# Kernel optimization log

Measured on AMD Instinct MI355X. Metric: run time of the kernel, lower is better.

## Reference

```python
import jax, jax.numpy as jnp
import numpy as np

N = 524288      # total nodes across batched subgraphs
E = 4194304     # total edges (avg degree ~8)
B = 4096        # number of subgraphs (links)
H = 32          # hidden_dim
L = 3           # num_layers
K = 30          # sort-pool k
MAXZ = 1000     # max DRNL label
EPS = 1e-5      # BatchNorm eps


def setup_inputs() -> dict:
    key = jax.random.key(0)
    ks = jax.random.split(key, 12)
    x_z = jax.random.randint(ks[0], (N,), 0, MAXZ + 1, dtype=jnp.int32)
    edge_index = jax.random.randint(ks[1], (2, E), 0, N, dtype=jnp.int32)
    batch = jnp.sort(jax.random.randint(ks[2], (N,), 0, B, dtype=jnp.int32))
    # parameters
    emb = jax.random.normal(ks[3], (MAXZ + 1, H), jnp.float32) * 0.1
    Wc = jax.random.normal(ks[4], (L, H, H), jnp.float32) * (1.0 / np.sqrt(H))
    bc = jnp.zeros((L, H), jnp.float32)
    gamma = jnp.ones((L, H), jnp.float32)
    beta = jnp.zeros((L, H), jnp.float32)
    rmean = jax.random.normal(ks[5], (L, H), jnp.float32) * 0.1
    rvar = 1.0 + 0.1 * jax.random.uniform(ks[6], (L, H), jnp.float32)
    W1 = jax.random.normal(ks[7], (K * H, H), jnp.float32) * (1.0 / np.sqrt(K * H))
    b1 = jnp.zeros((H,), jnp.float32)
    W2 = jax.random.normal(ks[8], (H, H // 2), jnp.float32) * (1.0 / np.sqrt(H))
    b2 = jnp.zeros((H // 2,), jnp.float32)
    W3 = jax.random.normal(ks[9], (H // 2, 1), jnp.float32) * (1.0 / np.sqrt(H // 2))
    b3 = jnp.zeros((1,), jnp.float32)
    return dict(x_z=x_z, edge_index=edge_index, batch=batch, emb=emb, Wc=Wc, bc=bc,
                gamma=gamma, beta=beta, rmean=rmean, rvar=rvar,
                W1=W1, b1=b1, W2=W2, b2=b2, W3=W3, b3=b3)


def reference(x_z, edge_index, batch, emb, Wc, bc, gamma, beta, rmean, rvar,
              W1, b1, W2, b2, W3, b3):
    src, dst = edge_index[0], edge_index[1]
    # GCN symmetric normalization with added self-loops: deg[i] = in_deg(i) + 1
    deg = jnp.zeros((N,), jnp.float32).at[dst].add(1.0) + 1.0
    dinv = jax.lax.rsqrt(deg)
    enorm = dinv[src] * dinv[dst]          # [E]
    self_norm = dinv * dinv                # [N] self-loop coefficient

    x = emb[x_z]                           # [N, H]
    for i in range(L):
        h = x @ Wc[i]                      # [N, H]
        agg = (jnp.zeros_like(h).at[dst].add(h[src] * enorm[:, None])
               + h * self_norm[:, None] + bc[i])
        # BatchNorm1d (eval: running stats) + ReLU; dropout is identity in eval
        xn = (agg - rmean[i]) * jax.lax.rsqrt(rvar[i] + EPS) * gamma[i] + beta[i]
        x = jax.nn.relu(xn)

    # SortAggregation: per-graph sort desc by last channel, keep top-K, zero-pad
    order = jnp.lexsort((-x[:, -1], batch))   # group by graph, desc by last feat
    xs = x[order]
    bs = batch[order]
    counts = jnp.zeros((B,), jnp.int32).at[batch].add(1)
    starts = jnp.concatenate([jnp.zeros((1,), jnp.int32), jnp.cumsum(counts)[:-1]])
    rank = jnp.arange(N, dtype=jnp.int32) - starts[bs]
    slot = jnp.where(rank < K, rank, K)       # overflow -> dummy slot K
    pooled = jnp.zeros((B, K + 1, H), x.dtype).at[bs, slot].set(xs)
    pooled = pooled[:, :K].reshape(B, K * H)  # [B, K*H]

    h1 = jax.nn.relu(pooled @ W1 + b1)
    h2 = jax.nn.relu(h1 @ W2 + b2)
    out = (h2 @ W3 + b3)[:, 0]                # [B]
    return out
```

## Files before the change

### kernel.cpp

```cpp
#include <hip/hip_runtime.h>
#include <hip/hip_bf16.h>
#include <stdint.h>

#define N_NODES 524288
#define N_EDGES 4194304
#define N_GRAPHS 4096
#define HDIM 32
#define NLAYERS 3
#define KPOOL 30
#define MAXC 1024

#define NBUCKET 1024
#define BSHIFT 9
#define NPB 512
#define NCOPY 8
#define HIST_SZ (NBUCKET * NCOPY)
#define CAP 6144
#define EPB 16384
#define NBIN (N_EDGES / EPB)

typedef unsigned long long ull;


__global__ void k_hist(const int* __restrict__ dst, int* __restrict__ ghist,
                       int* __restrict__ gbh) {
    __shared__ int lh[NBUCKET];
    int t = threadIdx.x;
    for (int i = t; i < NBUCKET; i += 256) lh[i] = 0;
    __syncthreads();
    int base = blockIdx.x * EPB;
    for (int i = t; i < EPB; i += 256) {
        int d = dst[base + i];
        atomicAdd(&lh[d >> BSHIFT], 1);
    }
    __syncthreads();
    int c = blockIdx.x & 7;
    for (int i = t; i < NBUCKET; i += 256) {
        int v = lh[i];
        gbh[blockIdx.x * NBUCKET + i] = v;
        if (v) atomicAdd(&ghist[c * NBUCKET + i], v);
    }
}

__global__ void k_scan8k(const int* __restrict__ ghist, int* __restrict__ gbase,
                         int* __restrict__ cur) {
    __shared__ int tmp[256];
    int t = threadIdx.x;
    int loc[32];
    int s = 0;
    for (int k = 0; k < 32; ++k) {
        int r = t * 32 + k;
        int idx = (r & 7) * NBUCKET + (r >> 3);
        loc[k] = ghist[idx];
        s += loc[k];
    }
    tmp[t] = s;
    __syncthreads();
    for (int d = 1; d < 256; d <<= 1) {
        int a = (t >= d) ? tmp[t - d] : 0;
        __syncthreads();
        tmp[t] += a;
        __syncthreads();
    }
    int run = tmp[t] - s;
    for (int k = 0; k < 32; ++k) {
        int r = t * 32 + k;
        int idx = (r & 7) * NBUCKET + (r >> 3);
        gbase[idx] = run;
        cur[idx] = run;
        run += loc[k];
    }
}

__global__ void k_bin(const int* __restrict__ src, const int* __restrict__ dst,
                      int* __restrict__ cur, const int* __restrict__ gbh,
                      ull* __restrict__ stage) {
    __shared__ int lbase[NBUCKET];
    __shared__ int lcur[NBUCKET];
    int t = threadIdx.x;
    int c = blockIdx.x & 7;
    for (int i = t; i < NBUCKET; i += 256) {
        int v = gbh[blockIdx.x * NBUCKET + i];
        lbase[i] = v ? atomicAdd(&cur[c * NBUCKET + i], v) : 0;
        lcur[i] = 0;
    }
    __syncthreads();
    int base = blockIdx.x * EPB;
    for (int i = t; i < EPB; i += 256) {
        int e = base + i;
        int d = dst[e];
        int b = d >> BSHIFT;
        int off = atomicAdd(&lcur[b], 1);
        ull rec = ((ull)(unsigned)src[e] << 32)
                | (unsigned)(((d & (NPB - 1)) << 22) | e);
        stage[lbase[b] + off] = rec;
    }
}

__global__ void k_cnt(const ull* __restrict__ stage, const int* __restrict__ gbase,
                      float* __restrict__ dinv, int* __restrict__ offs,
                      int* __restrict__ perm) {
    __shared__ int cnt[NPB];
    __shared__ int tmp[256];
    int b = blockIdx.x, t = threadIdx.x;
    int s0 = gbase[b];
    int s1 = (b == NBUCKET - 1) ? N_EDGES : gbase[b + 1];
    int win = s1 - s0;
    for (int j = t; j < NPB; j += 256) cnt[j] = 0;
    __syncthreads();
    const unsigned* lo32 = (const unsigned*)stage;
    for (int i = t; i < win; i += 256) {
        unsigned k = lo32[2 * (s0 + i)];
        atomicAdd(&cnt[(k >> 22) & (NPB - 1)], 1);
    }
    __syncthreads();
    int j0 = 2 * t, j1 = 2 * t + 1;
    int a0 = cnt[j0], a1 = cnt[j1];
    {
        float d0 = (float)(a0 + 1);
        float q0 = (float)sqrt((double)d0);
        dinv[b * NPB + j0] = (float)(1.0 / (double)q0);
        float d1 = (float)(a1 + 1);
        float q1 = (float)sqrt((double)d1);
        dinv[b * NPB + j1] = (float)(1.0 / (double)q1);
    }
    int s = a0 + a1;
    tmp[t] = s;
    __syncthreads();
    for (int d = 1; d < 256; d <<= 1) {
        int a = (t >= d) ? tmp[t - d] : 0;
        __syncthreads();
        tmp[t] += a;
        __syncthreads();
    }
    int run = tmp[t] - s;
    offs[b * NPB + j0] = s0 + run;
    offs[b * NPB + j1] = s0 + run + a0;
    if (b == NBUCKET - 1 && t == 255) offs[N_NODES] = N_EDGES;
    __syncthreads();
    for (int jj = 0; jj < 2; ++jj) {
        int j = 2 * t + jj;
        int dj = cnt[j];
        int r = 0;
        for (int k = 0; k < NPB; ++k) {
            int dk = cnt[k];
            r += (dk < dj) || (dk == dj && k < j);
        }
        perm[b * NPB + r] = b * NPB + j;
    }
}

__global__ void k_build2(const ull* __restrict__ stage, const int* __restrict__ gbase,
                         const int* __restrict__ offs, const float* __restrict__ dinv,
                         ull* __restrict__ csr2) {
    __shared__ ull grp[CAP];
    __shared__ int sstart[NPB];
    __shared__ int scur[NPB];
    int b = blockIdx.x, t = threadIdx.x;
    int s0 = gbase[b];
    int s1 = (b == NBUCKET - 1) ? N_EDGES : gbase[b + 1];
    int win = s1 - s0;
    for (int j = t; j < NPB; j += 256) {
        int v = offs[b * NPB + j] - s0;
        sstart[j] = v;
        scur[j] = v;
    }
    __syncthreads();

    if (win <= CAP) {
        for (int i = t; i < win; i += 256) {
            ull v = stage[s0 + i];
            unsigned k = (unsigned)v;
            int pos = atomicAdd(&scur[(k >> 22) & (NPB - 1)], 1);
            grp[pos] = v;
        }
        __syncthreads();
        for (int jj = 0; jj < 2; ++jj) {
            int j = 2 * t + jj;
            int beg = sstart[j], end = scur[j];
            for (int i = beg + 1; i < end; ++i) {
                ull v = grp[i];
                unsigned kv = (unsigned)v;
                int q = i - 1;
                while (q >= beg && (unsigned)grp[q] > kv) { grp[q + 1] = grp[q]; --q; }
                grp[q + 1] = v;
            }
        }
        __syncthreads();
        int i = t;
        for (; i + 768 < win; i += 1024) {
            ull v0 = grp[i], v1 = grp[i + 256], v2 = grp[i + 512], v3 = grp[i + 768];
            float d0 = dinv[(int)(v0 >> 32)];
            float d1 = dinv[(int)(v1 >> 32)];
            float d2 = dinv[(int)(v2 >> 32)];
            float d3 = dinv[(int)(v3 >> 32)];
            csr2[s0 + i]       = (v0 & 0xffffffff00000000ull) | (unsigned)__float_as_uint(d0);
            csr2[s0 + i + 256] = (v1 & 0xffffffff00000000ull) | (unsigned)__float_as_uint(d1);
            csr2[s0 + i + 512] = (v2 & 0xffffffff00000000ull) | (unsigned)__float_as_uint(d2);
            csr2[s0 + i + 768] = (v3 & 0xffffffff00000000ull) | (unsigned)__float_as_uint(d3);
        }
        for (; i < win; i += 256) {
            ull v = grp[i];
            float dv = dinv[(int)(v >> 32)];
            csr2[s0 + i] = (v & 0xffffffff00000000ull) | (unsigned)__float_as_uint(dv);
        }
    } else {
        for (int i = t; i < win; i += 256) {
            ull v = stage[s0 + i];
            unsigned k = (unsigned)v;
            int pos = s0 + atomicAdd(&scur[(k >> 22) & (NPB - 1)], 1);
            csr2[pos] = v;
        }
        __syncthreads();
        for (int jj = 0; jj < 2; ++jj) {
            int j = 2 * t + jj;
            int beg = s0 + sstart[j], end = s0 + scur[j];
            for (int i = beg + 1; i < end; ++i) {
                ull v = csr2[i];
                unsigned kv = (unsigned)v;
                int q = i - 1;
                while (q >= beg && (unsigned)csr2[q] > kv) { csr2[q + 1] = csr2[q]; --q; }
                csr2[q + 1] = v;
            }
        }
        __syncthreads();
        for (int i = t; i < win; i += 256) {
            ull v = csr2[s0 + i];
            float dv = dinv[(int)(v >> 32)];
            csr2[s0 + i] = (v & 0xffffffff00000000ull) | (unsigned)__float_as_uint(dv);
        }
    }
}

__global__ void k_bnprep(const float* __restrict__ rvar, float* __restrict__ rs) {
    int i = threadIdx.x;
    if (i < NLAYERS * HDIM) {
        float rv = __fadd_rn(rvar[i], 1e-5f);
        float sq = (float)sqrt((double)rv);
        rs[i] = (float)(1.0 / (double)sq);
    }
}

__global__ void k_embed_mm(const int* __restrict__ xz, const float* __restrict__ emb,
                           const float* __restrict__ Wc, float* __restrict__ h) {
    __shared__ float Wl[HDIM * HDIM];
    __shared__ float xt[256];
    int t = threadIdx.x;
    int base = blockIdx.x * 256;
    for (int i = t; i < HDIM * HDIM; i += 256) Wl[i] = Wc[i];
    {
        int gid = base + t;
        int n = gid >> 5, c = gid & 31;
        xt[t] = emb[xz[n] * HDIM + c];
    }
    __syncthreads();
    int nl = t >> 5, c = t & 31;
    float acc = 0.0f;
#pragma unroll
    for (int k = 0; k < HDIM; ++k) acc = __fmaf_rn(xt[nl * HDIM + k], Wl[k * HDIM + c], acc);
    h[base + t] = acc;
}

__device__ __forceinline__ float agg_phase(const float* __restrict__ h,
                                           const float* __restrict__ dinv,
                                           const int* __restrict__ offs,
                                           const ull* __restrict__ csr2,
                                           const float* __restrict__ bc,
                                           const float* __restrict__ rmean,
                                           const float* __restrict__ rs,
                                           const float* __restrict__ gamma,
                                           const float* __restrict__ beta,
                                           int n, int c) {
    float di = dinv[n];
    float hself = h[n * HDIM + c];
    float accE = 0.0f;
    int beg = offs[n], end = offs[n + 1];
    int i = beg;
    for (; i + 8 <= end; i += 8) {
        ull r0 = csr2[i];
        ull r1 = csr2[i + 1];
        ull r2 = csr2[i + 2];
        ull r3 = csr2[i + 3];
        ull r4 = csr2[i + 4];
        ull r5 = csr2[i + 5];
        ull r6 = csr2[i + 6];
        ull r7 = csr2[i + 7];
        float h0 = h[(int)(r0 >> 32) * HDIM + c];
        float h1 = h[(int)(r1 >> 32) * HDIM + c];
        float h2 = h[(int)(r2 >> 32) * HDIM + c];
        float h3 = h[(int)(r3 >> 32) * HDIM + c];
        float h4 = h[(int)(r4 >> 32) * HDIM + c];
        float h5 = h[(int)(r5 >> 32) * HDIM + c];
        float h6 = h[(int)(r6 >> 32) * HDIM + c];
        float h7 = h[(int)(r7 >> 32) * HDIM + c];
        accE = __fadd_rn(accE, __fmul_rn(h0, __fmul_rn(__uint_as_float((unsigned)r0), di)));
        accE = __fadd_rn(accE, __fmul_rn(h1, __fmul_rn(__uint_as_float((unsigned)r1), di)));
        accE = __fadd_rn(accE, __fmul_rn(h2, __fmul_rn(__uint_as_float((unsigned)r2), di)));
        accE = __fadd_rn(accE, __fmul_rn(h3, __fmul_rn(__uint_as_float((unsigned)r3), di)));
        accE = __fadd_rn(accE, __fmul_rn(h4, __fmul_rn(__uint_as_float((unsigned)r4), di)));
        accE = __fadd_rn(accE, __fmul_rn(h5, __fmul_rn(__uint_as_float((unsigned)r5), di)));
        accE = __fadd_rn(accE, __fmul_rn(h6, __fmul_rn(__uint_as_float((unsigned)r6), di)));
        accE = __fadd_rn(accE, __fmul_rn(h7, __fmul_rn(__uint_as_float((unsigned)r7), di)));
    }
    for (; i + 4 <= end; i += 4) {
        ull r0 = csr2[i];
        ull r1 = csr2[i + 1];
        ull r2 = csr2[i + 2];
        ull r3 = csr2[i + 3];
        float h0 = h[(int)(r0 >> 32) * HDIM + c];
        float h1 = h[(int)(r1 >> 32) * HDIM + c];
        float h2 = h[(int)(r2 >> 32) * HDIM + c];
        float h3 = h[(int)(r3 >> 32) * HDIM + c];
        accE = __fadd_rn(accE, __fmul_rn(h0, __fmul_rn(__uint_as_float((unsigned)r0), di)));
        accE = __fadd_rn(accE, __fmul_rn(h1, __fmul_rn(__uint_as_float((unsigned)r1), di)));
        accE = __fadd_rn(accE, __fmul_rn(h2, __fmul_rn(__uint_as_float((unsigned)r2), di)));
        accE = __fadd_rn(accE, __fmul_rn(h3, __fmul_rn(__uint_as_float((unsigned)r3), di)));
    }
    for (; i < end; ++i) {
        ull r = csr2[i];
        float hv = h[(int)(r >> 32) * HDIM + c];
        float dv = __uint_as_float((unsigned)r);
        accE = __fadd_rn(accE, __fmul_rn(hv, __fmul_rn(dv, di)));
    }
    float sn = __fmul_rn(di, di);
    float t1 = __fmul_rn(hself, sn);
    float a2 = __fadd_rn(accE, t1);
    float a3 = __fadd_rn(a2, bc[c]);
    float tt = __fsub_rn(a3, rmean[c]);
    float u  = __fmul_rn(tt, rs[c]);
    float v  = __fmul_rn(u, gamma[c]);
    float xn = __fadd_rn(v, beta[c]);
    return (xn > 0.0f) ? xn : 0.0f;
}

__global__ void k_agg_mm(const float* __restrict__ h, const float* __restrict__ dinv,
                         const int* __restrict__ offs, const ull* __restrict__ csr2,
                         const int* __restrict__ perm,
                         const float* __restrict__ bc, const float* __restrict__ rmean,
                         const float* __restrict__ rs, const float* __restrict__ gamma,
                         const float* __restrict__ beta,
                         const float* __restrict__ Wnext, float* __restrict__ hout) {
    __shared__ float Wl[HDIM * HDIM];
    __shared__ float xt[256];
    __shared__ int nodes[8];
    int t = threadIdx.x;
    for (int i = t; i < HDIM * HDIM; i += 256) Wl[i] = Wnext[i];
    if (t < 8) nodes[t] = perm[blockIdx.x * 8 + t];
    __syncthreads();
    int slot = t >> 5, c = t & 31;
    int n = nodes[slot];
    xt[t] = agg_phase(h, dinv, offs, csr2, bc, rmean, rs, gamma, beta, n, c);
    __syncthreads();
    float acc = 0.0f;
#pragma unroll
    for (int k = 0; k < HDIM; ++k) acc = __fmaf_rn(xt[slot * HDIM + k], Wl[k * HDIM + c], acc);
    hout[n * HDIM + c] = acc;
}

__global__ void k_agg_last(const float* __restrict__ h, const float* __restrict__ dinv,
                           const int* __restrict__ offs, const ull* __restrict__ csr2,
                           const int* __restrict__ perm,
                           const float* __restrict__ bc, const float* __restrict__ rmean,
                           const float* __restrict__ rs, const float* __restrict__ gamma,
                           const float* __restrict__ beta, float* __restrict__ xout,
                           float* __restrict__ lastc) {
    __shared__ int nodes[8];
    int t = threadIdx.x;
    if (t < 8) nodes[t] = perm[blockIdx.x * 8 + t];
    __syncthreads();
    int slot = t >> 5, c = t & 31;
    int n = nodes[slot];
    float v = agg_phase(h, dinv, offs, csr2, bc, rmean, rs, gamma, beta, n, c);
    xout[n * HDIM + c] = v;
    if (c == 31) lastc[n] = v;
}

__global__ void k_starts(const int* __restrict__ batch, int* __restrict__ start) {
    int n = blockIdx.x * 256 + threadIdx.x;
    if (n >= N_NODES) return;
    int bn = batch[n];
    int bp = (n == 0) ? -1 : batch[n - 1];
    for (int g = bp + 1; g <= bn; ++g) start[g] = n;
    if (n == N_NODES - 1) {
        for (int g = bn + 1; g <= N_GRAPHS; ++g) start[g] = N_NODES;
    }
}

__global__ void k_pool_mlp(const float* __restrict__ x, const float* __restrict__ lastc,
                           const int* __restrict__ start,
                           const float* __restrict__ W1, const float* __restrict__ b1,
                           const float* __restrict__ W2, const float* __restrict__ b2,
                           const float* __restrict__ W3, const float* __restrict__ b3,
                           float* __restrict__ out) {
    int g = blockIdx.x;
    int t = threadIdx.x;
    int s = start[g], e = start[g + 1];
    int cnt = e - s;

    __shared__ ull keys[MAXC];
    __shared__ int sel[KPOOL];
    __shared__ float pl[KPOOL * HDIM];
    __shared__ double part[64];
    __shared__ double h1[HDIM];
    __shared__ double h2[HDIM / 2];

    bool inlds = (cnt <= MAXC);
    if (inlds) {
        for (int i = t; i < cnt; i += 64) {
            int n = s + i;
            keys[i] = ((ull)__float_as_uint(lastc[n]) << 32) | (unsigned int)(~n);
        }
    }
    __syncthreads();

    ull prev = ~0ull;
    for (int k = 0; k < KPOOL; ++k) {
        if (k < cnt) {
            ull best = 0ull;
            if (inlds) {
                for (int i = t; i < cnt; i += 64) {
                    ull key = keys[i];
                    if (key < prev && key > best) best = key;
                }
            } else {
                for (int n = s + t; n < e; n += 64) {
                    ull key = ((ull)__float_as_uint(lastc[n]) << 32) | (unsigned int)(~n);
                    if (key < prev && key > best) best = key;
                }
            }
            for (int off = 32; off; off >>= 1) {
                ull o = __shfl_down(best, off);
                if (o > best) best = o;
            }
            best = __shfl(best, 0);
            prev = best;
            if (t == 0) sel[k] = (int)(~((unsigned int)(best & 0xffffffffull)));
        } else {
            if (t == 0) sel[k] = -1;
        }
    }
    __syncthreads();

    for (int idx = t; idx < KPOOL * HDIM; idx += 64) {
        int k = idx >> 5, c = idx & 31;
        int n = sel[k];
        pl[idx] = (n >= 0) ? x[n * HDIM + c] : 0.0f;
    }
    __syncthreads();

    {
        int j = t & 31;
        int half = t >> 5;
        double acc = 0.0;
        int r0 = half * (KPOOL * HDIM / 2);
        for (int r = r0; r < r0 + KPOOL * HDIM / 2; ++r)
            acc += (double)pl[r] * (double)W1[r * HDIM + j];
        part[t] = acc;
    }
    __syncthreads();
    if (t < HDIM) {
        double v = part[t] + part[t + 32] + (double)b1[t];
        h1[t] = (v > 0.0) ? v : 0.0;
    }
    __syncthreads();

    if (t < HDIM / 2) {
        double a2 = (double)b2[t];
        for (int i = 0; i < HDIM; ++i) a2 += h1[i] * (double)W2[i * (HDIM / 2) + t];
        h2[t] = (a2 > 0.0) ? a2 : 0.0;
    }
    __syncthreads();

    if (t == 0) {
        double o = (double)b3[0];
        for (int i = 0; i < HDIM / 2; ++i) o += h2[i] * (double)W3[i];
        out[g] = (float)o;
    }
}

extern "C" void kernel_launch(void* const* d_in, const int* in_sizes, int n_in,
                              void* d_out, int out_size, void* d_ws, size_t ws_size,
                              hipStream_t stream) {
    const int*   xz    = (const int*)d_in[0];
    const int*   src   = (const int*)d_in[1];
    const int*   dst   = (const int*)d_in[1] + N_EDGES;
    const int*   batch = (const int*)d_in[2];
    const float* emb   = (const float*)d_in[3];
    const float* Wc    = (const float*)d_in[4];
    const float* bc    = (const float*)d_in[5];
    const float* gamma = (const float*)d_in[6];
    const float* beta  = (const float*)d_in[7];
    const float* rmean = (const float*)d_in[8];
    const float* rvar  = (const float*)d_in[9];
    const float* W1    = (const float*)d_in[10];
    const float* b1    = (const float*)d_in[11];
    const float* W2    = (const float*)d_in[12];
    const float* b2    = (const float*)d_in[13];
    const float* W3    = (const float*)d_in[14];
    const float* b3    = (const float*)d_in[15];
    float* out = (float*)d_out;

    char* p = (char*)d_ws;
    auto carve = [&](size_t bytes) {
        void* q = (void*)p;
        p += (bytes + 255) & ~size_t(255);
        return q;
    };
    int*   ghist = (int*)carve(HIST_SZ * 4);
    int*   gbase = (int*)carve(HIST_SZ * 4);
    int*   cur   = (int*)carve(HIST_SZ * 4);
    int*   gbh   = (int*)carve((size_t)NBIN * NBUCKET * 4);
    ull*   stage = (ull*)carve((size_t)N_EDGES * 8);
    ull*   csr2  = (ull*)carve((size_t)N_EDGES * 8);
    float* dinv  = (float*)carve(N_NODES * 4);
    int*   offs  = (int*)carve((N_NODES + 1) * 4);
    int*   permB = (int*)carve(N_NODES * 4);
    int*   start = (int*)carve((N_GRAPHS + 1) * 4);
    float* rs    = (float*)carve(NLAYERS * HDIM * 4);
    float* lastc = (float*)carve(N_NODES * 4);
    float* bufA  = (float*)carve((size_t)N_NODES * HDIM * 4);
    float* bufB  = (float*)carve((size_t)N_NODES * HDIM * 4);

    hipMemsetAsync(ghist, 0, HIST_SZ * 4, stream);

    k_hist<<<NBIN, 256, 0, stream>>>(dst, ghist, gbh);
    k_scan8k<<<1, 256, 0, stream>>>(ghist, gbase, cur);
    k_bin<<<NBIN, 256, 0, stream>>>(src, dst, cur, gbh, stage);
    k_cnt<<<NBUCKET, 256, 0, stream>>>(stage, gbase, dinv, offs, permB);
    k_build2<<<NBUCKET, 256, 0, stream>>>(stage, gbase, offs, dinv, csr2);
    k_bnprep<<<1, 128, 0, stream>>>(rvar, rs);
    k_starts<<<N_NODES / 256, 256, 0, stream>>>(batch, start);

    const int NG = (N_NODES * HDIM) / 256;
    k_embed_mm<<<NG, 256, 0, stream>>>(xz, emb, Wc + 0 * HDIM * HDIM, bufA);
    k_agg_mm<<<N_NODES / 8, 256, 0, stream>>>(bufA, dinv, offs, csr2, permB,
        bc + 0 * HDIM, rmean + 0 * HDIM, rs + 0 * HDIM, gamma + 0 * HDIM, beta + 0 * HDIM,
        Wc + 1 * HDIM * HDIM, bufB);
    k_agg_mm<<<N_NODES / 8, 256, 0, stream>>>(bufB, dinv, offs, csr2, permB,
        bc + 1 * HDIM, rmean + 1 * HDIM, rs + 1 * HDIM, gamma + 1 * HDIM, beta + 1 * HDIM,
        Wc + 2 * HDIM * HDIM, bufA);
    k_agg_last<<<N_NODES / 8, 256, 0, stream>>>(bufA, dinv, offs, csr2, permB,
        bc + 2 * HDIM, rmean + 2 * HDIM, rs + 2 * HDIM, gamma + 2 * HDIM, beta + 2 * HDIM,
        bufB, lastc);

    k_pool_mlp<<<N_GRAPHS, 64, 0, stream>>>(bufB, lastc, start, W1, b1, W2, b2, W3, b3, out);
}
```

Measured before the change: 1.032 ms.

## Fuse small preprocessing kernels, split staging into SoA, add nontemporal accesses

Merges k_starts and k_bnprep into the histogram launch and the embedding matmul into the binning launch, which removes several kernel launches and lets independent work share the GPU. The 64-bit stage buffer is split into separate lo/hi arrays so k_cnt reads only the 32-bit key. The source index is stored pre-multiplied by 128, the row stride in bytes, which saves an address multiply in the gather. Nontemporal loads and stores are added on streaming CSR reads and output writes. This adds branch-divergent mixed-role blocks, and the byte-offset packing assumes src*128 fits in 32 bits.

```diff
diff --git a/kernel.cpp b/kernel.cpp
--- a/kernel.cpp
+++ b/kernel.cpp
@@ -18,27 +18,48 @@
 #define CAP 6144
 #define EPB 16384
 #define NBIN (N_EDGES / EPB)
+#define NG ((N_NODES * HDIM) / 256)
+#define NSTART (N_NODES / 256)
 
 typedef unsigned long long ull;
 
 
 __global__ void k_hist(const int* __restrict__ dst, int* __restrict__ ghist,
-                       int* __restrict__ gbh) {
+                       int* __restrict__ gbh,
+                       const int* __restrict__ batch, int* __restrict__ start,
+                       const float* __restrict__ rvar, float* __restrict__ rs) {
     __shared__ int lh[NBUCKET];
     int t = threadIdx.x;
-    for (int i = t; i < NBUCKET; i += 256) lh[i] = 0;
-    __syncthreads();
-    int base = blockIdx.x * EPB;
-    for (int i = t; i < EPB; i += 256) {
-        int d = dst[base + i];
-        atomicAdd(&lh[d >> BSHIFT], 1);
-    }
-    __syncthreads();
-    int c = blockIdx.x & 7;
-    for (int i = t; i < NBUCKET; i += 256) {
-        int v = lh[i];
-        gbh[blockIdx.x * NBUCKET + i] = v;
-        if (v) atomicAdd(&ghist[c * NBUCKET + i], v);
+    int blk = blockIdx.x;
+    if (blk < NBIN) {
+        for (int i = t; i < NBUCKET; i += 256) lh[i] = 0;
+        __syncthreads();
+        int base = blk * EPB;
+        for (int i = t; i < EPB; i += 256) {
+            int d = dst[base + i];
+            atomicAdd(&lh[d >> BSHIFT], 1);
+        }
+        __syncthreads();
+        int c = blk & 7;
+        for (int i = t; i < NBUCKET; i += 256) {
+            int v = lh[i];
+            gbh[blk * NBUCKET + i] = v;
+            if (v) atomicAdd(&ghist[c * NBUCKET + i], v);
+        }
+    } else if (blk < NBIN + NSTART) {
+        int n = (blk - NBIN) * 256 + t;
+        int bn = batch[n];
+        int bp = (n == 0) ? -1 : batch[n - 1];
+        for (int g = bp + 1; g <= bn; ++g) start[g] = n;
+        if (n == N_NODES - 1) {
+            for (int g = bn + 1; g <= N_GRAPHS; ++g) start[g] = N_NODES;
+        }
+    } else {
+        if (t < NLAYERS * HDIM) {
+            float rv = __fadd_rn(rvar[t], 1e-5f);
+            float sq = (float)sqrt((double)rv);
+            rs[t] = (float)(1.0 / (double)sq);
+        }
     }
 }
 
@@ -72,32 +93,55 @@
     }
 }
 
-__global__ void k_bin(const int* __restrict__ src, const int* __restrict__ dst,
-                      int* __restrict__ cur, const int* __restrict__ gbh,
-                      ull* __restrict__ stage) {
-    __shared__ int lbase[NBUCKET];
-    __shared__ int lcur[NBUCKET];
+__global__ void k_binembed(const int* __restrict__ src, const int* __restrict__ dst,
+                           int* __restrict__ cur, const int* __restrict__ gbh,
+                           unsigned* __restrict__ stageLo, unsigned* __restrict__ stageHi,
+                           const int* __restrict__ xz, const float* __restrict__ emb,
+                           const float* __restrict__ Wc, float* __restrict__ h) {
+    __shared__ int smem[2048];
     int t = threadIdx.x;
-    int c = blockIdx.x & 7;
-    for (int i = t; i < NBUCKET; i += 256) {
-        int v = gbh[blockIdx.x * NBUCKET + i];
-        lbase[i] = v ? atomicAdd(&cur[c * NBUCKET + i], v) : 0;
-        lcur[i] = 0;
-    }
-    __syncthreads();
-    int base = blockIdx.x * EPB;
-    for (int i = t; i < EPB; i += 256) {
-        int e = base + i;
-        int d = dst[e];
-        int b = d >> BSHIFT;
-        int off = atomicAdd(&lcur[b], 1);
-        ull rec = ((ull)(unsigned)src[e] << 32)
-                | (unsigned)(((d & (NPB - 1)) << 22) | e);
-        stage[lbase[b] + off] = rec;
-    }
-}
-
-__global__ void k_cnt(const ull* __restrict__ stage, const int* __restrict__ gbase,
+    int blk = blockIdx.x;
+    if (blk < NBIN) {
+        int* lbase = smem;
+        int* lcur  = smem + NBUCKET;
+        int c = blk & 7;
+        for (int i = t; i < NBUCKET; i += 256) {
+            int v = gbh[blk * NBUCKET + i];
+            lbase[i] = v ? atomicAdd(&cur[c * NBUCKET + i], v) : 0;
+            lcur[i] = 0;
+        }
+        __syncthreads();
+        int base = blk * EPB;
+        for (int i = t; i < EPB; i += 256) {
+            int e = base + i;
+            int d = dst[e];
+            int b = d >> BSHIFT;
+            int off = atomicAdd(&lcur[b], 1);
+            int pos = lbase[b] + off;
+            stageLo[pos] = (unsigned)(((d & (NPB - 1)) << 22) | e);
+            stageHi[pos] = (unsigned)src[e];
+        }
+    } else {
+        float* Wl = (float*)smem;
+        float* xt = (float*)(smem + 1024);
+        int base = (blk - NBIN) * 256;
+        for (int i = t; i < HDIM * HDIM; i += 256) Wl[i] = Wc[i];
+        {
+            int gid = base + t;
+            int n = gid >> 5, c = gid & 31;
+            xt[t] = emb[xz[n] * HDIM + c];
+        }
+        __syncthreads();
+        int nl = t >> 5, c = t & 31;
+        float acc = 0.0f;
+#pragma unroll
+        for (int k = 0; k < HDIM; ++k)
+            acc = __fmaf_rn(xt[nl * HDIM + k], Wl[k * HDIM + c], acc);
+        h[base + t] = acc;
+    }
+}
+
+__global__ void k_cnt(const unsigned* __restrict__ stageLo, const int* __restrict__ gbase,
                       float* __restrict__ dinv, int* __restrict__ offs,
                       int* __restrict__ perm) {
     __shared__ int cnt[NPB];
@@ -108,9 +152,8 @@
     int win = s1 - s0;
     for (int j = t; j < NPB; j += 256) cnt[j] = 0;
     __syncthreads();
-    const unsigned* lo32 = (const unsigned*)stage;
     for (int i = t; i < win; i += 256) {
-        unsigned k = lo32[2 * (s0 + i)];
+        unsigned k = __builtin_nontemporal_load(&stageLo[s0 + i]);
         atomicAdd(&cnt[(k >> 22) & (NPB - 1)], 1);
     }
     __syncthreads();
@@ -150,7 +193,9 @@
     }
 }
 
-__global__ void k_build2(const ull* __restrict__ stage, const int* __restrict__ gbase,
+__global__ void k_build2(const unsigned* __restrict__ stageLo,
+                         const unsigned* __restrict__ stageHi,
+                         const int* __restrict__ gbase,
                          const int* __restrict__ offs, const float* __restrict__ dinv,
                          ull* __restrict__ csr2) {
     __shared__ ull grp[CAP];
@@ -169,10 +214,10 @@
 
     if (win <= CAP) {
         for (int i = t; i < win; i += 256) {
-            ull v = stage[s0 + i];
-            unsigned k = (unsigned)v;
-            int pos = atomicAdd(&scur[(k >> 22) & (NPB - 1)], 1);
-            grp[pos] = v;
+            unsigned lo = __builtin_nontemporal_load(&stageLo[s0 + i]);
+            unsigned hi = __builtin_nontemporal_load(&stageHi[s0 + i]);
+            int pos = atomicAdd(&scur[(lo >> 22) & (NPB - 1)], 1);
+            grp[pos] = ((ull)(hi << 7) << 32) | lo;
         }
         __syncthreads();
         for (int jj = 0; jj < 2; ++jj) {
@@ -190,10 +235,10 @@
         int i = t;
         for (; i + 768 < win; i += 1024) {
             ull v0 = grp[i], v1 = grp[i + 256], v2 = grp[i + 512], v3 = grp[i + 768];
-            float d0 = dinv[(int)(v0 >> 32)];
-            float d1 = dinv[(int)(v1 >> 32)];
-            float d2 = dinv[(int)(v2 >> 32)];
-            float d3 = dinv[(int)(v3 >> 32)];
+            float d0 = dinv[(unsigned)(v0 >> 32) >> 7];
+            float d1 = dinv[(unsigned)(v1 >> 32) >> 7];
+            float d2 = dinv[(unsigned)(v2 >> 32) >> 7];
+            float d3 = dinv[(unsigned)(v3 >> 32) >> 7];
             csr2[s0 + i]       = (v0 & 0xffffffff00000000ull) | (unsigned)__float_as_uint(d0);
             csr2[s0 + i + 256] = (v1 & 0xffffffff00000000ull) | (unsigned)__float_as_uint(d1);
             csr2[s0 + i + 512] = (v2 & 0xffffffff00000000ull) | (unsigned)__float_as_uint(d2);
@@ -201,15 +246,15 @@
         }
         for (; i < win; i += 256) {
             ull v = grp[i];
-            float dv = dinv[(int)(v >> 32)];
+            float dv = dinv[(unsigned)(v >> 32) >> 7];
             csr2[s0 + i] = (v & 0xffffffff00000000ull) | (unsigned)__float_as_uint(dv);
         }
     } else {
         for (int i = t; i < win; i += 256) {
-            ull v = stage[s0 + i];
-            unsigned k = (unsigned)v;
-            int pos = s0 + atomicAdd(&scur[(k >> 22) & (NPB - 1)], 1);
-            csr2[pos] = v;
+            unsigned lo = stageLo[s0 + i];
+            unsigned hi = stageHi[s0 + i];
+            int pos = s0 + atomicAdd(&scur[(lo >> 22) & (NPB - 1)], 1);
+            csr2[pos] = ((ull)(hi << 7) << 32) | lo;
         }
         __syncthreads();
         for (int jj = 0; jj < 2; ++jj) {
@@ -226,39 +271,10 @@
         __syncthreads();
         for (int i = t; i < win; i += 256) {
             ull v = csr2[s0 + i];
-            float dv = dinv[(int)(v >> 32)];
+            float dv = dinv[(unsigned)(v >> 32) >> 7];
             csr2[s0 + i] = (v & 0xffffffff00000000ull) | (unsigned)__float_as_uint(dv);
         }
     }
-}
-
-__global__ void k_bnprep(const float* __restrict__ rvar, float* __restrict__ rs) {
-    int i = threadIdx.x;
-    if (i < NLAYERS * HDIM) {
-        float rv = __fadd_rn(rvar[i], 1e-5f);
-        float sq = (float)sqrt((double)rv);
-        rs[i] = (float)(1.0 / (double)sq);
-    }
-}
-
-__global__ void k_embed_mm(const int* __restrict__ xz, const float* __restrict__ emb,
-                           const float* __restrict__ Wc, float* __restrict__ h) {
-    __shared__ float Wl[HDIM * HDIM];
-    __shared__ float xt[256];
-    int t = threadIdx.x;
-    int base = blockIdx.x * 256;
-    for (int i = t; i < HDIM * HDIM; i += 256) Wl[i] = Wc[i];
-    {
-        int gid = base + t;
-        int n = gid >> 5, c = gid & 31;
-        xt[t] = emb[xz[n] * HDIM + c];
-    }
-    __syncthreads();
-    int nl = t >> 5, c = t & 31;
-    float acc = 0.0f;
-#pragma unroll
-    for (int k = 0; k < HDIM; ++k) acc = __fmaf_rn(xt[nl * HDIM + k], Wl[k * HDIM + c], acc);
-    h[base + t] = acc;
 }
 
 __device__ __forceinline__ float agg_phase(const float* __restrict__ h,
@@ -271,28 +287,30 @@
                                            const float* __restrict__ gamma,
                                            const float* __restrict__ beta,
                                            int n, int c) {
+    const char* hb = (const char*)h;
+    unsigned c4 = (unsigned)(c << 2);
     float di = dinv[n];
     float hself = h[n * HDIM + c];
     float accE = 0.0f;
     int beg = offs[n], end = offs[n + 1];
     int i = beg;
     for (; i + 8 <= end; i += 8) {
-        ull r0 = csr2[i];
-        ull r1 = csr2[i + 1];
-        ull r2 = csr2[i + 2];
-        ull r3 = csr2[i + 3];
-        ull r4 = csr2[i + 4];
-        ull r5 = csr2[i + 5];
-        ull r6 = csr2[i + 6];
-        ull r7 = csr2[i + 7];
-        float h0 = h[(int)(r0 >> 32) * HDIM + c];
-        float h1 = h[(int)(r1 >> 32) * HDIM + c];
-        float h2 = h[(int)(r2 >> 32) * HDIM + c];
-        float h3 = h[(int)(r3 >> 32) * HDIM + c];
-        float h4 = h[(int)(r4 >> 32) * HDIM + c];
-        float h5 = h[(int)(r5 >> 32) * HDIM + c];
-        float h6 = h[(int)(r6 >> 32) * HDIM + c];
-        float h7 = h[(int)(r7 >> 32) * HDIM + c];
+        ull r0 = __builtin_nontemporal_load(&csr2[i]);
+        ull r1 = __builtin_nontemporal_load(&csr2[i + 1]);
+        ull r2 = __builtin_nontemporal_load(&csr2[i + 2]);
+        ull r3 = __builtin_nontemporal_load(&csr2[i + 3]);
+        ull r4 = __builtin_nontemporal_load(&csr2[i + 4]);
+        ull r5 = __builtin_nontemporal_load(&csr2[i + 5]);
+        ull r6 = __builtin_nontemporal_load(&csr2[i + 6]);
+        ull r7 = __builtin_nontemporal_load(&csr2[i + 7]);
+        float h0 = *(const float*)(hb + ((unsigned)(r0 >> 32) + c4));
+        float h1 = *(const float*)(hb + ((unsigned)(r1 >> 32) + c4));
+        float h2 = *(const float*)(hb + ((unsigned)(r2 >> 32) + c4));
+        float h3 = *(const float*)(hb + ((unsigned)(r3 >> 32) + c4));
+        float h4 = *(const float*)(hb + ((unsigned)(r4 >> 32) + c4));
+        float h5 = *(const float*)(hb + ((unsigned)(r5 >> 32) + c4));
+        float h6 = *(const float*)(hb + ((unsigned)(r6 >> 32) + c4));
+        float h7 = *(const float*)(hb + ((unsigned)(r7 >> 32) + c4));
         accE = __fadd_rn(accE, __fmul_rn(h0, __fmul_rn(__uint_as_float((unsigned)r0), di)));
         accE = __fadd_rn(accE, __fmul_rn(h1, __fmul_rn(__uint_as_float((unsigned)r1), di)));
         accE = __fadd_rn(accE, __fmul_rn(h2, __fmul_rn(__uint_as_float((unsigned)r2), di)));
@@ -303,22 +321,22 @@
         accE = __fadd_rn(accE, __fmul_rn(h7, __fmul_rn(__uint_as_float((unsigned)r7), di)));
     }
     for (; i + 4 <= end; i += 4) {
-        ull r0 = csr2[i];
-        ull r1 = csr2[i + 1];
-        ull r2 = csr2[i + 2];
-        ull r3 = csr2[i + 3];
-        float h0 = h[(int)(r0 >> 32) * HDIM + c];
-        float h1 = h[(int)(r1 >> 32) * HDIM + c];
-        float h2 = h[(int)(r2 >> 32) * HDIM + c];
-        float h3 = h[(int)(r3 >> 32) * HDIM + c];
+        ull r0 = __builtin_nontemporal_load(&csr2[i]);
+        ull r1 = __builtin_nontemporal_load(&csr2[i + 1]);
+        ull r2 = __builtin_nontemporal_load(&csr2[i + 2]);
+        ull r3 = __builtin_nontemporal_load(&csr2[i + 3]);
+        float h0 = *(const float*)(hb + ((unsigned)(r0 >> 32) + c4));
+        float h1 = *(const float*)(hb + ((unsigned)(r1 >> 32) + c4));
+        float h2 = *(const float*)(hb + ((unsigned)(r2 >> 32) + c4));
+        float h3 = *(const float*)(hb + ((unsigned)(r3 >> 32) + c4));
         accE = __fadd_rn(accE, __fmul_rn(h0, __fmul_rn(__uint_as_float((unsigned)r0), di)));
         accE = __fadd_rn(accE, __fmul_rn(h1, __fmul_rn(__uint_as_float((unsigned)r1), di)));
         accE = __fadd_rn(accE, __fmul_rn(h2, __fmul_rn(__uint_as_float((unsigned)r2), di)));
         accE = __fadd_rn(accE, __fmul_rn(h3, __fmul_rn(__uint_as_float((unsigned)r3), di)));
     }
     for (; i < end; ++i) {
-        ull r = csr2[i];
-        float hv = h[(int)(r >> 32) * HDIM + c];
+        ull r = __builtin_nontemporal_load(&csr2[i]);
+        float hv = *(const float*)(hb + ((unsigned)(r >> 32) + c4));
         float dv = __uint_as_float((unsigned)r);
         accE = __fadd_rn(accE, __fmul_rn(hv, __fmul_rn(dv, di)));
     }
@@ -354,7 +372,7 @@
     float acc = 0.0f;
 #pragma unroll
     for (int k = 0; k < HDIM; ++k) acc = __fmaf_rn(xt[slot * HDIM + k], Wl[k * HDIM + c], acc);
-    hout[n * HDIM + c] = acc;
+    __builtin_nontemporal_store(acc, &hout[n * HDIM + c]);
 }
 
 __global__ void k_agg_last(const float* __restrict__ h, const float* __restrict__ dinv,
@@ -371,19 +389,8 @@
     int slot = t >> 5, c = t & 31;
     int n = nodes[slot];
     float v = agg_phase(h, dinv, offs, csr2, bc, rmean, rs, gamma, beta, n, c);
-    xout[n * HDIM + c] = v;
+    __builtin_nontemporal_store(v, &xout[n * HDIM + c]);
     if (c == 31) lastc[n] = v;
-}
-
-__global__ void k_starts(const int* __restrict__ batch, int* __restrict__ start) {
-    int n = blockIdx.x * 256 + threadIdx.x;
-    if (n >= N_NODES) return;
-    int bn = batch[n];
-    int bp = (n == 0) ? -1 : batch[n - 1];
-    for (int g = bp + 1; g <= bn; ++g) start[g] = n;
-    if (n == N_NODES - 1) {
-        for (int g = bn + 1; g <= N_GRAPHS; ++g) start[g] = N_NODES;
-    }
 }
 
 __global__ void k_pool_mlp(const float* __restrict__ x, const float* __restrict__ lastc,
@@ -506,33 +513,31 @@
         p += (bytes + 255) & ~size_t(255);
         return q;
     };
-    int*   ghist = (int*)carve(HIST_SZ * 4);
-    int*   gbase = (int*)carve(HIST_SZ * 4);
-    int*   cur   = (int*)carve(HIST_SZ * 4);
-    int*   gbh   = (int*)carve((size_t)NBIN * NBUCKET * 4);
-    ull*   stage = (ull*)carve((size_t)N_EDGES * 8);
-    ull*   csr2  = (ull*)carve((size_t)N_EDGES * 8);
-    float* dinv  = (float*)carve(N_NODES * 4);
-    int*   offs  = (int*)carve((N_NODES + 1) * 4);
-    int*   permB = (int*)carve(N_NODES * 4);
-    int*   start = (int*)carve((N_GRAPHS + 1) * 4);
-    float* rs    = (float*)carve(NLAYERS * HDIM * 4);
-    float* lastc = (float*)carve(N_NODES * 4);
-    float* bufA  = (float*)carve((size_t)N_NODES * HDIM * 4);
-    float* bufB  = (float*)carve((size_t)N_NODES * HDIM * 4);
+    int*      ghist   = (int*)carve(HIST_SZ * 4);
+    int*      gbase   = (int*)carve(HIST_SZ * 4);
+    int*      cur     = (int*)carve(HIST_SZ * 4);
+    int*      gbh     = (int*)carve((size_t)NBIN * NBUCKET * 4);
+    unsigned* stageLo = (unsigned*)carve((size_t)N_EDGES * 4);
+    unsigned* stageHi = (unsigned*)carve((size_t)N_EDGES * 4);
+    ull*      csr2    = (ull*)carve((size_t)N_EDGES * 8);
+    float*    dinv    = (float*)carve(N_NODES * 4);
+    int*      offs    = (int*)carve((N_NODES + 1) * 4);
+    int*      permB   = (int*)carve(N_NODES * 4);
+    int*      start   = (int*)carve((N_GRAPHS + 1) * 4);
+    float*    rs      = (float*)carve(NLAYERS * HDIM * 4);
+    float*    lastc   = (float*)carve(N_NODES * 4);
+    float*    bufA    = (float*)carve((size_t)N_NODES * HDIM * 4);
+    float*    bufB    = (float*)carve((size_t)N_NODES * HDIM * 4);
 
     hipMemsetAsync(ghist, 0, HIST_SZ * 4, stream);
 
-    k_hist<<<NBIN, 256, 0, stream>>>(dst, ghist, gbh);
+    k_hist<<<NBIN + NSTART + 1, 256, 0, stream>>>(dst, ghist, gbh, batch, start, rvar, rs);
     k_scan8k<<<1, 256, 0, stream>>>(ghist, gbase, cur);
-    k_bin<<<NBIN, 256, 0, stream>>>(src, dst, cur, gbh, stage);
-    k_cnt<<<NBUCKET, 256, 0, stream>>>(stage, gbase, dinv, offs, permB);
-    k_build2<<<NBUCKET, 256, 0, stream>>>(stage, gbase, offs, dinv, csr2);
-    k_bnprep<<<1, 128, 0, stream>>>(rvar, rs);
-    k_starts<<<N_NODES / 256, 256, 0, stream>>>(batch, start);
-
-    const int NG = (N_NODES * HDIM) / 256;
-    k_embed_mm<<<NG, 256, 0, stream>>>(xz, emb, Wc + 0 * HDIM * HDIM, bufA);
+    k_binembed<<<NBIN + NG, 256, 0, stream>>>(src, dst, cur, gbh, stageLo, stageHi,
+                                              xz, emb, Wc + 0 * HDIM * HDIM, bufA);
+    k_cnt<<<NBUCKET, 256, 0, stream>>>(stageLo, gbase, dinv, offs, permB);
+    k_build2<<<NBUCKET, 256, 0, stream>>>(stageLo, stageHi, gbase, offs, dinv, csr2);
+
     k_agg_mm<<<N_NODES / 8, 256, 0, stream>>>(bufA, dinv, offs, csr2, permB,
         bc + 0 * HDIM, rmean + 0 * HDIM, rs + 0 * HDIM, gamma + 0 * HDIM, beta + 0 * HDIM,
         Wc + 1 * HDIM * HDIM, bufB);
```

Result: slower. 1.178 ms (+14.2%).
